# Optimization experiments

Hardware: AMD Instinct MI355X
Metric: run time of the kernel (lower is better)

The kernel has to match this reference:

```python
import jax, jax.numpy as jnp
import numpy as np

SWIGLU_ALPHA = 1.702
SWIGLU_LIMIT = 7.0
B, S, H, E, K, I = 2, 2048, 2048, 32, 4, 1024


def setup_inputs() -> dict:
    key = jax.random.key(0)
    ks = jax.random.split(key, 8)
    return {
        "hidden_states": jax.random.normal(ks[0], (B, S, H), jnp.float32),
        "gate_w": jax.random.normal(ks[1], (E, H), jnp.float32) * 0.02,
        "gate_b": jnp.zeros((E,), jnp.float32),
        "w_gate": jax.random.normal(ks[2], (E, H, I), jnp.float32) * 0.02,
        "b_gate": jnp.zeros((E, I), jnp.float32),
        "w_up": jax.random.normal(ks[3], (E, H, I), jnp.float32) * 0.02,
        "b_up": jnp.zeros((E, I), jnp.float32),
        "w_down": jax.random.normal(ks[4], (E, I, H), jnp.float32) * 0.02,
        "b_down": jnp.zeros((E, H), jnp.float32),
    }


def reference(hidden_states, gate_w, gate_b, w_gate, b_gate, w_up, b_up, w_down, b_down):
    Bb, Ss, Hh = hidden_states.shape
    x = hidden_states.reshape(-1, Hh)                      # [T, H]
    # --- gate: top-k logits first, then softmax over the selected subset ---
    logits = x @ gate_w.T + gate_b                         # [T, E]
    topk_logits, topk_idx = jax.lax.top_k(logits, K)       # sorted descending
    topk_weight = jax.nn.softmax(topk_logits.astype(jnp.float32), axis=-1)  # [T, K]
    # --- dispatch: replicate each token K times, sort by expert id ---
    flat_idx = topk_idx.reshape(-1)                        # [T*K]
    xs = jnp.repeat(x, K, axis=0)                          # [T*K, H]
    order = jnp.argsort(flat_idx)                          # stable sort by expert
    xt = xs[order]
    gid = flat_idx[order]                                  # expert id per sorted row
    group_sizes = jnp.bincount(flat_idx, length=E).astype(jnp.int32)
    # --- grouped GEMM experts with GPT-OSS SwiGLU ---
    gate = jax.lax.ragged_dot(xt, w_gate, group_sizes) + b_gate[gid]
    up = jax.lax.ragged_dot(xt, w_up, group_sizes) + b_up[gid]
    gate = jnp.minimum(gate, SWIGLU_LIMIT)
    up = jnp.clip(up, -SWIGLU_LIMIT, SWIGLU_LIMIT)
    glu = gate * jax.nn.sigmoid(SWIGLU_ALPHA * gate)
    activated = (up + 1.0) * glu
    outs = jax.lax.ragged_dot(activated, w_down, group_sizes) + b_down[gid]
    # --- unsort and combine with routing weights ---
    inv = jnp.argsort(order)
    outs = outs[inv].reshape(-1, K, Hh)                    # [T, K, H]
    y = jnp.sum(outs * topk_weight[..., None], axis=1).astype(x.dtype)
    return y.reshape(Bb, Ss, Hh)
```

## Files before the change

### kernel.cpp

```cpp
#include <hip/hip_runtime.h>

#define T_TOK 4096
#define E_EXP 32
#define HDIM  2048
#define IDIM  1024
#define TKROW 16384
#define BM    256
#define MAXT  96

typedef __attribute__((ext_vector_type(8))) short   short8;
typedef __attribute__((ext_vector_type(8))) __bf16  bf16x8;
typedef __attribute__((ext_vector_type(4))) float   f32x4;

typedef const __attribute__((address_space(1))) unsigned int* gas_t;
typedef __attribute__((address_space(3))) unsigned int*       las_t;

static __device__ __forceinline__ void gload16(const void* g, void* l) {
    __builtin_amdgcn_global_load_lds((gas_t)(uintptr_t)g, (las_t)(uintptr_t)l, 16, 0, 0);
}

static __device__ __forceinline__ f32x4 mfma16(short8 a, short8 b, f32x4 c) {
    return __builtin_amdgcn_mfma_f32_16x16x32_bf16(
        __builtin_bit_cast(bf16x8, a), __builtin_bit_cast(bf16x8, b), c, 0, 0, 0);
}

static __device__ __forceinline__ unsigned short f2bf(float f) {
    unsigned u = __builtin_bit_cast(unsigned, f);
    unsigned r = (u + 0x7FFFu + ((u >> 16) & 1u)) >> 16;
    return (unsigned short)r;
}
static __device__ __forceinline__ float bf2f(unsigned short u) {
    return __builtin_bit_cast(float, ((unsigned)u) << 16);
}
static __device__ __forceinline__ unsigned cvtpk(float lo, float hi) {
    unsigned r;
    asm("v_cvt_pk_bf16_f32 %0, %1, %2" : "=v"(r) : "v"(lo), "v"(hi));
    return r;
}

#define VM0()   asm volatile("s_waitcnt vmcnt(0)" ::: "memory")
#define LGKM0() asm volatile("s_waitcnt lgkmcnt(0)" ::: "memory")

__global__ __launch_bounds__(256) void gating_kernel(
    const float* __restrict__ x, const float* __restrict__ gw,
    const float* __restrict__ gb, int* __restrict__ topk_idx,
    float* __restrict__ topk_w)
{
    int wave = threadIdx.x >> 6, lane = threadIdx.x & 63;
    int t = blockIdx.x * 4 + wave;
    const float* xr = x + (size_t)t * HDIM;
    float xv[32];
#pragma unroll
    for (int j = 0; j < 32; j++) xv[j] = xr[lane + 64 * j];
    float logits[E_EXP];
#pragma unroll
    for (int e = 0; e < E_EXP; e++) {
        const float* wr = gw + (size_t)e * HDIM;
        float s = 0.f;
#pragma unroll
        for (int j = 0; j < 32; j++) s = fmaf(xv[j], wr[lane + 64 * j], s);
#pragma unroll
        for (int off = 32; off; off >>= 1) s += __shfl_xor(s, off);
        logits[e] = s + gb[e];
    }
    unsigned sel = 0;
    float v[4]; int id[4];
#pragma unroll
    for (int kk = 0; kk < 4; kk++) {
        float best = -3.4e38f; int bi = 0;
#pragma unroll
        for (int e = 0; e < E_EXP; e++) {
            bool ok = ((sel >> e) & 1u) == 0u;
            bool gt = ok && (logits[e] > best);
            best = gt ? logits[e] : best;
            bi   = gt ? e : bi;
        }
        sel |= 1u << bi; v[kk] = best; id[kk] = bi;
    }
    float m0 = v[0];
    float e0 = __expf(v[0] - m0), e1 = __expf(v[1] - m0);
    float e2 = __expf(v[2] - m0), e3 = __expf(v[3] - m0);
    float inv = 1.f / (e0 + e1 + e2 + e3);
    if (lane == 0) {
        int b4 = t * 4;
        topk_idx[b4 + 0] = id[0]; topk_w[b4 + 0] = e0 * inv;
        topk_idx[b4 + 1] = id[1]; topk_w[b4 + 1] = e1 * inv;
        topk_idx[b4 + 2] = id[2]; topk_w[b4 + 2] = e2 * inv;
        topk_idx[b4 + 3] = id[3]; topk_w[b4 + 3] = e3 * inv;
    }
}

__global__ void init_kernel(int* counts, int* fill) {
    if (threadIdx.x < E_EXP) { counts[threadIdx.x] = 0; fill[threadIdx.x] = 0; }
}

__global__ void histo_kernel(const int* __restrict__ idx, int* counts) {
    int i = blockIdx.x * 256 + threadIdx.x;
    atomicAdd(&counts[idx[i]], 1);
}

__global__ void scan_tiles_kernel(const int* counts, int* offsets,
                                  int* tile_e, int* tile_r, int* ntiles) {
    if (threadIdx.x == 0) {
        int acc = 0;
        for (int e = 0; e < E_EXP; e++) { offsets[e] = acc; acc += counts[e]; }
        offsets[E_EXP] = acc;
        int nt = 0;
        for (int e = 0; e < E_EXP; e++) {
            int c = counts[e];
            for (int r = 0; r < c; r += BM) {
                tile_e[nt] = e; tile_r[nt] = offsets[e] + r; nt++;
            }
        }
        ntiles[0] = nt;
    }
}

__global__ void scatter_kernel(const int* __restrict__ idx, const int* __restrict__ offsets,
                               int* fill, int* __restrict__ pos_of, int* __restrict__ row_tok) {
    int i = blockIdx.x * 256 + threadIdx.x;
    int e = idx[i];
    int pos = offsets[e] + atomicAdd(&fill[e], 1);
    pos_of[i] = pos;
    row_tok[pos] = i >> 2;
}

__global__ __launch_bounds__(64) void gather_kernel(
    const float* __restrict__ x, const int* __restrict__ row_tok,
    unsigned short* __restrict__ xt)
{
    int r = blockIdx.x, lane = threadIdx.x;
    const f32x4* src = (const f32x4*)(x + (size_t)row_tok[r] * HDIM);
    unsigned short* dst = xt + (size_t)r * HDIM;
#pragma unroll
    for (int j = 0; j < 8; j++) {
        f32x4 f = src[lane + 64 * j];
        uint2 o;
        o.x = cvtpk(f[0], f[1]);
        o.y = cvtpk(f[2], f[3]);
        *(uint2*)(dst + 4 * (lane + 64 * j)) = o;
    }
}

__global__ __launch_bounds__(512, 2) void gemm1_kernel(
    const unsigned short* __restrict__ xt, const float* __restrict__ w_gate,
    const float* __restrict__ b_gate, const float* __restrict__ w_up,
    const float* __restrict__ b_up, const int* __restrict__ tile_e,
    const int* __restrict__ tile_r, const int* __restrict__ ntiles,
    const int* __restrict__ offsets, const int* __restrict__ counts,
    unsigned short* __restrict__ act)
{
    __shared__ unsigned short As[2][BM * 64];
    __shared__ unsigned short Bgs[2][128 * 64];
    __shared__ unsigned short Bus[2][128 * 64];

    int t = threadIdx.x, lane = t & 63, w = t >> 6;
    int wr = w >> 2, wc = w & 3;
    int lrow = lane & 15, lg8 = (lane >> 4) * 8;

    int arow_l = (lane >> 3);
    int achunk = (lane & 7) ^ arow_l;
    int bn = (t & 31) * 4, bk = (t >> 5) * 4;
    int bfswz = ((t & 31) & 7) << 3;

    int nt = ntiles[0];
    int nitems = nt * 8;

    for (int item = blockIdx.x; item < nitems; item += gridDim.x) {
        int tid = item % nt, nb = item / nt;
        int e = tile_e[tid], row0 = tile_r[tid];
        int cnt_end = offsets[e] + counts[e];
        int n0 = nb * 128;

        f32x4 accg[8][2], accu[8][2];
#pragma unroll
        for (int m = 0; m < 8; m++)
#pragma unroll
            for (int n = 0; n < 2; n++) { accg[m][n] = (f32x4)0.f; accu[m][n] = (f32x4)0.f; }

        size_t wB = (size_t)e * ((size_t)HDIM * IDIM) + (size_t)bk * IDIM + n0 + bn;
        f32x4 gReg[4], uReg[4];

#define G1_STAGE_A(KT, BUF) do { int k0_ = (KT) * 64; \
    _Pragma("unroll") for (int i_ = 0; i_ < 4; i_++) { \
        int ar_ = row0 + 32 * w + 8 * i_ + arow_l; \
        if (ar_ > TKROW - 1) ar_ = TKROW - 1; \
        gload16(xt + (size_t)ar_ * HDIM + k0_ + achunk * 8, \
                (void*)&As[BUF][(32 * w + 8 * i_) * 64]); \
    } } while (0)

#define G1_LOADB(KT) do { \
    const float* gp_ = w_gate + wB + (size_t)(KT) * 64 * IDIM; \
    const float* up_ = w_up   + wB + (size_t)(KT) * 64 * IDIM; \
    _Pragma("unroll") for (int kk_ = 0; kk_ < 4; kk_++) { \
        gReg[kk_] = *(const f32x4*)(gp_ + (size_t)kk_ * IDIM); \
        uReg[kk_] = *(const f32x4*)(up_ + (size_t)kk_ * IDIM); \
    } } while (0)

#define G1_WRITEB(BUF) do { \
    _Pragma("unroll") for (int j_ = 0; j_ < 4; j_++) { \
        uint2 vg_, vu_; \
        vg_.x = cvtpk(gReg[0][j_], gReg[1][j_]); vg_.y = cvtpk(gReg[2][j_], gReg[3][j_]); \
        vu_.x = cvtpk(uReg[0][j_], uReg[1][j_]); vu_.y = cvtpk(uReg[2][j_], uReg[3][j_]); \
        int d_ = (bn + j_) * 64 + (bk ^ bfswz); \
        *(uint2*)&Bgs[BUF][d_] = vg_; *(uint2*)&Bus[BUF][d_] = vu_; \
    } } while (0)

#define G1_MFMA(BUF) do { \
    __builtin_amdgcn_s_setprio(1); \
    _Pragma("unroll") for (int kk_ = 0; kk_ < 2; kk_++) { \
        short8 af_[8], bg_[2], bu_[2]; \
        int ke_ = kk_ * 32 + lg8; \
        _Pragma("unroll") for (int m_ = 0; m_ < 8; m_++) \
            af_[m_] = *(const short8*)&As[BUF][(wr * 128 + m_ * 16 + lrow) * 64 + (ke_ ^ ((lrow & 7) << 3))]; \
        _Pragma("unroll") for (int n_ = 0; n_ < 2; n_++) { \
            int rb_ = wc * 32 + n_ * 16 + lrow; \
            int d_ = rb_ * 64 + (ke_ ^ (((rb_ >> 2) & 7) << 3)); \
            bg_[n_] = *(const short8*)&Bgs[BUF][d_]; \
            bu_[n_] = *(const short8*)&Bus[BUF][d_]; \
        } \
        _Pragma("unroll") for (int m_ = 0; m_ < 8; m_++) \
        _Pragma("unroll") for (int n_ = 0; n_ < 2; n_++) { \
            accg[m_][n_] = mfma16(af_[m_], bg_[n_], accg[m_][n_]); \
            accu[m_][n_] = mfma16(af_[m_], bu_[n_], accu[m_][n_]); \
        } \
    } \
    __builtin_amdgcn_s_setprio(0); } while (0)

        G1_STAGE_A(0, 0);
        G1_LOADB(0);
        VM0();
        G1_WRITEB(0);
        LGKM0();
        __builtin_amdgcn_s_barrier();

        int cur = 0;
#pragma unroll 1
        for (int kt = 0; kt < 32; kt++) {
            if (kt + 1 < 32) { G1_STAGE_A(kt + 1, cur ^ 1); G1_LOADB(kt + 1); }
            G1_MFMA(cur);
            VM0();
            if (kt + 1 < 32) G1_WRITEB(cur ^ 1);
            LGKM0();
            __builtin_amdgcn_s_barrier();
            cur ^= 1;
        }
#undef G1_STAGE_A
#undef G1_LOADB
#undef G1_WRITEB
#undef G1_MFMA

#pragma unroll
        for (int nf = 0; nf < 2; nf++) {
            int col = n0 + wc * 32 + nf * 16 + lrow;
            float bgv = b_gate[e * IDIM + col];
            float buv = b_up[e * IDIM + col];
#pragma unroll
            for (int m = 0; m < 8; m++) {
                int rb = row0 + wr * 128 + m * 16 + (lane >> 4) * 4;
#pragma unroll
                for (int r = 0; r < 4; r++) {
                    int grow = rb + r;
                    if (grow < cnt_end) {
                        float gv = accg[m][nf][r] + bgv;
                        float uv = accu[m][nf][r] + buv;
                        gv = fminf(gv, 7.f);
                        uv = fminf(fmaxf(uv, -7.f), 7.f);
                        float glu = gv / (1.f + __expf(-1.702f * gv));
                        act[(size_t)grow * IDIM + col] = f2bf((uv + 1.f) * glu);
                    }
                }
            }
        }
        __builtin_amdgcn_s_barrier();
    }
}

__global__ __launch_bounds__(512, 2) void gemm2_kernel(
    const unsigned short* __restrict__ actb, const float* __restrict__ w_down,
    const float* __restrict__ b_down, const int* __restrict__ tile_e,
    const int* __restrict__ tile_r, const int* __restrict__ ntiles,
    const int* __restrict__ offsets, const int* __restrict__ counts,
    unsigned short* __restrict__ outs)
{
    __shared__ unsigned short As[2][BM * 64];
    __shared__ unsigned short Bs[2][256 * 64];

    int t = threadIdx.x, lane = t & 63, w = t >> 6;
    int wr = w >> 2, wc = w & 3;
    int lrow = lane & 15, lg8 = (lane >> 4) * 8;

    int arow_l = (lane >> 3);
    int achunk = (lane & 7) ^ arow_l;
    int bn = (t & 63) * 4, bk = w * 8;
    int bfswz = (lane & 7) << 3;

    int nt = ntiles[0];
    int nitems = nt * 8;

    for (int item = blockIdx.x; item < nitems; item += gridDim.x) {
        int tid = item % nt, nb = item / nt;
        int e = tile_e[tid], row0 = tile_r[tid];
        int cnt_end = offsets[e] + counts[e];
        int n0 = nb * 256;

        f32x4 acc[8][4];
#pragma unroll
        for (int m = 0; m < 8; m++)
#pragma unroll
            for (int n = 0; n < 4; n++) acc[m][n] = (f32x4)0.f;

        size_t wB = (size_t)e * ((size_t)IDIM * HDIM) + (size_t)bk * HDIM + n0 + bn;
        f32x4 dReg[8];

#define G2_STAGE_A(KT, BUF) do { int k0_ = (KT) * 64; \
    _Pragma("unroll") for (int i_ = 0; i_ < 4; i_++) { \
        int ar_ = row0 + 32 * w + 8 * i_ + arow_l; \
        if (ar_ > TKROW - 1) ar_ = TKROW - 1; \
        gload16(actb + (size_t)ar_ * IDIM + k0_ + achunk * 8, \
                (void*)&As[BUF][(32 * w + 8 * i_) * 64]); \
    } } while (0)

#define G2_LOADB(KT) do { \
    const float* gp_ = w_down + wB + (size_t)(KT) * 64 * HDIM; \
    _Pragma("unroll") for (int kk_ = 0; kk_ < 8; kk_++) \
        dReg[kk_] = *(const f32x4*)(gp_ + (size_t)kk_ * HDIM); \
    } while (0)

#define G2_WRITEB(BUF) do { \
    _Pragma("unroll") for (int j_ = 0; j_ < 4; j_++) { \
        uint4 v_; \
        v_.x = cvtpk(dReg[0][j_], dReg[1][j_]); v_.y = cvtpk(dReg[2][j_], dReg[3][j_]); \
        v_.z = cvtpk(dReg[4][j_], dReg[5][j_]); v_.w = cvtpk(dReg[6][j_], dReg[7][j_]); \
        int d_ = (bn + j_) * 64 + (bk ^ bfswz); \
        *(uint4*)&Bs[BUF][d_] = v_; \
    } } while (0)

#define G2_MFMA(BUF) do { \
    __builtin_amdgcn_s_setprio(1); \
    _Pragma("unroll") for (int kk_ = 0; kk_ < 2; kk_++) { \
        short8 af_[8], bf_[4]; \
        int ke_ = kk_ * 32 + lg8; \
        _Pragma("unroll") for (int m_ = 0; m_ < 8; m_++) \
            af_[m_] = *(const short8*)&As[BUF][(wr * 128 + m_ * 16 + lrow) * 64 + (ke_ ^ ((lrow & 7) << 3))]; \
        _Pragma("unroll") for (int n_ = 0; n_ < 4; n_++) { \
            int rb_ = wc * 64 + n_ * 16 + lrow; \
            bf_[n_] = *(const short8*)&Bs[BUF][rb_ * 64 + (ke_ ^ (((rb_ >> 2) & 7) << 3))]; \
        } \
        _Pragma("unroll") for (int m_ = 0; m_ < 8; m_++) \
        _Pragma("unroll") for (int n_ = 0; n_ < 4; n_++) \
            acc[m_][n_] = mfma16(af_[m_], bf_[n_], acc[m_][n_]); \
    } \
    __builtin_amdgcn_s_setprio(0); } while (0)

        G2_STAGE_A(0, 0);
        G2_LOADB(0);
        VM0();
        G2_WRITEB(0);
        LGKM0();
        __builtin_amdgcn_s_barrier();

        int cur = 0;
#pragma unroll 1
        for (int kt = 0; kt < 16; kt++) {
            if (kt + 1 < 16) { G2_STAGE_A(kt + 1, cur ^ 1); G2_LOADB(kt + 1); }
            G2_MFMA(cur);
            VM0();
            if (kt + 1 < 16) G2_WRITEB(cur ^ 1);
            LGKM0();
            __builtin_amdgcn_s_barrier();
            cur ^= 1;
        }
#undef G2_STAGE_A
#undef G2_LOADB
#undef G2_WRITEB
#undef G2_MFMA

#pragma unroll
        for (int nf = 0; nf < 4; nf++) {
            int col = n0 + wc * 64 + nf * 16 + lrow;
            float bdv = b_down[e * HDIM + col];
#pragma unroll
            for (int m = 0; m < 8; m++) {
                int rb = row0 + wr * 128 + m * 16 + (lane >> 4) * 4;
#pragma unroll
                for (int r = 0; r < 4; r++) {
                    int grow = rb + r;
                    if (grow < cnt_end)
                        outs[(size_t)grow * HDIM + col] = f2bf(acc[m][nf][r] + bdv);
                }
            }
        }
        __builtin_amdgcn_s_barrier();
    }
}

__global__ __launch_bounds__(256) void combine_kernel(
    const unsigned short* __restrict__ outs, const int* __restrict__ pos_of,
    const float* __restrict__ topk_w, float* __restrict__ y)
{
    int tok = blockIdx.x;
    int c0 = threadIdx.x * 8;
    float acc[8] = {0.f, 0.f, 0.f, 0.f, 0.f, 0.f, 0.f, 0.f};
#pragma unroll
    for (int k = 0; k < 4; k++) {
        int pos = pos_of[tok * 4 + k];
        float w = topk_w[tok * 4 + k];
        short8 vv = *(const short8*)(outs + (size_t)pos * HDIM + c0);
#pragma unroll
        for (int j = 0; j < 8; j++)
            acc[j] = fmaf(w, bf2f((unsigned short)vv[j]), acc[j]);
    }
    float4 o0 = make_float4(acc[0], acc[1], acc[2], acc[3]);
    float4 o1 = make_float4(acc[4], acc[5], acc[6], acc[7]);
    *(float4*)(y + (size_t)tok * HDIM + c0)     = o0;
    *(float4*)(y + (size_t)tok * HDIM + c0 + 4) = o1;
}

extern "C" void kernel_launch(void* const* d_in, const int* in_sizes, int n_in,
                              void* d_out, int out_size, void* d_ws, size_t ws_size,
                              hipStream_t stream) {
    const float* x      = (const float*)d_in[0];
    const float* gw     = (const float*)d_in[1];
    const float* gb     = (const float*)d_in[2];
    const float* w_gate = (const float*)d_in[3];
    const float* b_gate = (const float*)d_in[4];
    const float* w_up   = (const float*)d_in[5];
    const float* b_up   = (const float*)d_in[6];
    const float* w_down = (const float*)d_in[7];
    const float* b_down = (const float*)d_in[8];
    float* y = (float*)d_out;

    char* base = (char*)d_ws;
    size_t off = 0;
    int*   topk_idx = (int*)(base + off);   off += (size_t)TKROW * 4;
    float* topk_w   = (float*)(base + off); off += (size_t)TKROW * 4;
    int*   counts   = (int*)(base + off);   off += 256;
    int*   offsets  = (int*)(base + off);   off += 256;
    int*   fill     = (int*)(base + off);   off += 256;
    int*   ntiles   = (int*)(base + off);   off += 256;
    int*   tile_e   = (int*)(base + off);   off += 1024;
    int*   tile_r   = (int*)(base + off);   off += 1024;
    int*   pos_of   = (int*)(base + off);   off += (size_t)TKROW * 4;
    int*   row_tok  = (int*)(base + off);   off += (size_t)TKROW * 4;
    unsigned short* xt   = (unsigned short*)(base + off); off += (size_t)TKROW * HDIM * 2;
    unsigned short* act  = (unsigned short*)(base + off); off += (size_t)TKROW * IDIM * 2;
    unsigned short* outs = (unsigned short*)(base + off); off += (size_t)TKROW * HDIM * 2;

    init_kernel<<<1, 64, 0, stream>>>(counts, fill);
    gating_kernel<<<T_TOK / 4, 256, 0, stream>>>(x, gw, gb, topk_idx, topk_w);
    histo_kernel<<<TKROW / 256, 256, 0, stream>>>(topk_idx, counts);
    scan_tiles_kernel<<<1, 64, 0, stream>>>(counts, offsets, tile_e, tile_r, ntiles);
    scatter_kernel<<<TKROW / 256, 256, 0, stream>>>(topk_idx, offsets, fill, pos_of, row_tok);
    gather_kernel<<<TKROW, 64, 0, stream>>>(x, row_tok, xt);
    gemm1_kernel<<<256, 512, 0, stream>>>(
        xt, w_gate, b_gate, w_up, b_up, tile_e, tile_r, ntiles, offsets, counts, act);
    gemm2_kernel<<<256, 512, 0, stream>>>(
        act, w_down, b_down, tile_e, tile_r, ntiles, offsets, counts, outs);
    combine_kernel<<<T_TOK, 256, 0, stream>>>(outs, pos_of, topk_w, y);
}
```

Measured before the change: 709.0 us.

## Replace persistent grid-stride GEMM loops with a precomputed XCD-aware worklist grid

```diff
diff --git a/kernel.cpp b/kernel.cpp
--- a/kernel.cpp
+++ b/kernel.cpp
@@ -7,6 +7,7 @@
 #define TKROW 16384
 #define BM    256
 #define MAXT  96
+#define WLY   160
 
 typedef __attribute__((ext_vector_type(8))) short   short8;
 typedef __attribute__((ext_vector_type(8))) __bf16  bf16x8;
@@ -100,19 +101,39 @@
 }
 
 __global__ void scan_tiles_kernel(const int* counts, int* offsets,
-                                  int* tile_e, int* tile_r, int* ntiles) {
-    if (threadIdx.x == 0) {
+                                  int* tile_e, int* tile_r, int* ntiles, int* wl) {
+    int t = threadIdx.x;
+    for (int i = t; i < 8 * WLY; i += 64) wl[i] = -1;
+    __syncthreads();
+    if (t == 0) {
         int acc = 0;
+        int tstart[E_EXP + 1];
         for (int e = 0; e < E_EXP; e++) { offsets[e] = acc; acc += counts[e]; }
         offsets[E_EXP] = acc;
         int nt = 0;
         for (int e = 0; e < E_EXP; e++) {
+            tstart[e] = nt;
             int c = counts[e];
             for (int r = 0; r < c; r += BM) {
                 tile_e[nt] = e; tile_r[nt] = offsets[e] + r; nt++;
             }
         }
+        tstart[E_EXP] = nt;
         ntiles[0] = nt;
+        int cnt[8];
+        for (int i = 0; i < 8; i++) cnt[i] = 0;
+        for (int nb = 0; nb < 8; nb++) {
+            for (int e = 0; e < E_EXP; e++) {
+                int ntl = tstart[e + 1] - tstart[e];
+                if (ntl == 0) continue;
+                int best = 0;
+                for (int xc = 1; xc < 8; xc++) if (cnt[xc] < cnt[best]) best = xc;
+                for (int k = 0; k < ntl && cnt[best] < WLY; k++) {
+                    wl[cnt[best] * 8 + best] = ((tstart[e] + k) << 3) | nb;
+                    cnt[best]++;
+                }
+            }
+        }
     }
 }
 
@@ -146,10 +167,17 @@
     const unsigned short* __restrict__ xt, const float* __restrict__ w_gate,
     const float* __restrict__ b_gate, const float* __restrict__ w_up,
     const float* __restrict__ b_up, const int* __restrict__ tile_e,
-    const int* __restrict__ tile_r, const int* __restrict__ ntiles,
+    const int* __restrict__ tile_r, const int* __restrict__ wl,
     const int* __restrict__ offsets, const int* __restrict__ counts,
     unsigned short* __restrict__ act)
 {
+    int item = wl[blockIdx.y * 8 + blockIdx.x];
+    if (item < 0) return;
+    int tid = item >> 3, nb = item & 7;
+    int e = tile_e[tid], row0 = tile_r[tid];
+    int cnt_end = offsets[e] + counts[e];
+    int n0 = nb * 128;
+
     __shared__ unsigned short As[2][BM * 64];
     __shared__ unsigned short Bgs[2][128 * 64];
     __shared__ unsigned short Bus[2][128 * 64];
@@ -157,29 +185,20 @@
     int t = threadIdx.x, lane = t & 63, w = t >> 6;
     int wr = w >> 2, wc = w & 3;
     int lrow = lane & 15, lg8 = (lane >> 4) * 8;
+
+    f32x4 accg[8][2], accu[8][2];
+#pragma unroll
+    for (int m = 0; m < 8; m++)
+#pragma unroll
+        for (int n = 0; n < 2; n++) { accg[m][n] = (f32x4)0.f; accu[m][n] = (f32x4)0.f; }
 
     int arow_l = (lane >> 3);
     int achunk = (lane & 7) ^ arow_l;
     int bn = (t & 31) * 4, bk = (t >> 5) * 4;
     int bfswz = ((t & 31) & 7) << 3;
-
-    int nt = ntiles[0];
-    int nitems = nt * 8;
-
-    for (int item = blockIdx.x; item < nitems; item += gridDim.x) {
-        int tid = item % nt, nb = item / nt;
-        int e = tile_e[tid], row0 = tile_r[tid];
-        int cnt_end = offsets[e] + counts[e];
-        int n0 = nb * 128;
-
-        f32x4 accg[8][2], accu[8][2];
-#pragma unroll
-        for (int m = 0; m < 8; m++)
-#pragma unroll
-            for (int n = 0; n < 2; n++) { accg[m][n] = (f32x4)0.f; accu[m][n] = (f32x4)0.f; }
-
-        size_t wB = (size_t)e * ((size_t)HDIM * IDIM) + (size_t)bk * IDIM + n0 + bn;
-        f32x4 gReg[4], uReg[4];
+    size_t wB = (size_t)e * ((size_t)HDIM * IDIM) + (size_t)bk * IDIM + n0 + bn;
+
+    f32x4 gReg[4], uReg[4];
 
 #define G1_STAGE_A(KT, BUF) do { int k0_ = (KT) * 64; \
     _Pragma("unroll") for (int i_ = 0; i_ < 4; i_++) { \
@@ -227,91 +246,87 @@
     } \
     __builtin_amdgcn_s_setprio(0); } while (0)
 
-        G1_STAGE_A(0, 0);
-        G1_LOADB(0);
+    G1_STAGE_A(0, 0);
+    G1_LOADB(0);
+    VM0();
+    G1_WRITEB(0);
+    LGKM0();
+    __builtin_amdgcn_s_barrier();
+
+    int cur = 0;
+#pragma unroll 1
+    for (int kt = 0; kt < 32; kt++) {
+        if (kt + 1 < 32) { G1_STAGE_A(kt + 1, cur ^ 1); G1_LOADB(kt + 1); }
+        G1_MFMA(cur);
         VM0();
-        G1_WRITEB(0);
+        if (kt + 1 < 32) G1_WRITEB(cur ^ 1);
         LGKM0();
         __builtin_amdgcn_s_barrier();
-
-        int cur = 0;
-#pragma unroll 1
-        for (int kt = 0; kt < 32; kt++) {
-            if (kt + 1 < 32) { G1_STAGE_A(kt + 1, cur ^ 1); G1_LOADB(kt + 1); }
-            G1_MFMA(cur);
-            VM0();
-            if (kt + 1 < 32) G1_WRITEB(cur ^ 1);
-            LGKM0();
-            __builtin_amdgcn_s_barrier();
-            cur ^= 1;
-        }
+        cur ^= 1;
+    }
 #undef G1_STAGE_A
 #undef G1_LOADB
 #undef G1_WRITEB
 #undef G1_MFMA
 
 #pragma unroll
-        for (int nf = 0; nf < 2; nf++) {
-            int col = n0 + wc * 32 + nf * 16 + lrow;
-            float bgv = b_gate[e * IDIM + col];
-            float buv = b_up[e * IDIM + col];
-#pragma unroll
-            for (int m = 0; m < 8; m++) {
-                int rb = row0 + wr * 128 + m * 16 + (lane >> 4) * 4;
-#pragma unroll
-                for (int r = 0; r < 4; r++) {
-                    int grow = rb + r;
-                    if (grow < cnt_end) {
-                        float gv = accg[m][nf][r] + bgv;
-                        float uv = accu[m][nf][r] + buv;
-                        gv = fminf(gv, 7.f);
-                        uv = fminf(fmaxf(uv, -7.f), 7.f);
-                        float glu = gv / (1.f + __expf(-1.702f * gv));
-                        act[(size_t)grow * IDIM + col] = f2bf((uv + 1.f) * glu);
-                    }
+    for (int nf = 0; nf < 2; nf++) {
+        int col = n0 + wc * 32 + nf * 16 + lrow;
+        float bgv = b_gate[e * IDIM + col];
+        float buv = b_up[e * IDIM + col];
+#pragma unroll
+        for (int m = 0; m < 8; m++) {
+            int rb = row0 + wr * 128 + m * 16 + (lane >> 4) * 4;
+#pragma unroll
+            for (int r = 0; r < 4; r++) {
+                int grow = rb + r;
+                if (grow < cnt_end) {
+                    float gv = accg[m][nf][r] + bgv;
+                    float uv = accu[m][nf][r] + buv;
+                    gv = fminf(gv, 7.f);
+                    uv = fminf(fmaxf(uv, -7.f), 7.f);
+                    float glu = gv / (1.f + __expf(-1.702f * gv));
+                    act[(size_t)grow * IDIM + col] = f2bf((uv + 1.f) * glu);
                 }
             }
         }
-        __builtin_amdgcn_s_barrier();
     }
 }
 
 __global__ __launch_bounds__(512, 2) void gemm2_kernel(
     const unsigned short* __restrict__ actb, const float* __restrict__ w_down,
     const float* __restrict__ b_down, const int* __restrict__ tile_e,
-    const int* __restrict__ tile_r, const int* __restrict__ ntiles,
+    const int* __restrict__ tile_r, const int* __restrict__ wl,
     const int* __restrict__ offsets, const int* __restrict__ counts,
     unsigned short* __restrict__ outs)
 {
+    int item = wl[blockIdx.y * 8 + blockIdx.x];
+    if (item < 0) return;
+    int tid = item >> 3, nb = item & 7;
+    int e = tile_e[tid], row0 = tile_r[tid];
+    int cnt_end = offsets[e] + counts[e];
+    int n0 = nb * 256;
+
     __shared__ unsigned short As[2][BM * 64];
     __shared__ unsigned short Bs[2][256 * 64];
 
     int t = threadIdx.x, lane = t & 63, w = t >> 6;
     int wr = w >> 2, wc = w & 3;
     int lrow = lane & 15, lg8 = (lane >> 4) * 8;
+
+    f32x4 acc[8][4];
+#pragma unroll
+    for (int m = 0; m < 8; m++)
+#pragma unroll
+        for (int n = 0; n < 4; n++) acc[m][n] = (f32x4)0.f;
 
     int arow_l = (lane >> 3);
     int achunk = (lane & 7) ^ arow_l;
     int bn = (t & 63) * 4, bk = w * 8;
     int bfswz = (lane & 7) << 3;
-
-    int nt = ntiles[0];
-    int nitems = nt * 8;
-
-    for (int item = blockIdx.x; item < nitems; item += gridDim.x) {
-        int tid = item % nt, nb = item / nt;
-        int e = tile_e[tid], row0 = tile_r[tid];
-        int cnt_end = offsets[e] + counts[e];
-        int n0 = nb * 256;
-
-        f32x4 acc[8][4];
-#pragma unroll
-        for (int m = 0; m < 8; m++)
-#pragma unroll
-            for (int n = 0; n < 4; n++) acc[m][n] = (f32x4)0.f;
-
-        size_t wB = (size_t)e * ((size_t)IDIM * HDIM) + (size_t)bk * HDIM + n0 + bn;
-        f32x4 dReg[8];
+    size_t wB = (size_t)e * ((size_t)IDIM * HDIM) + (size_t)bk * HDIM + n0 + bn;
+
+    f32x4 dReg[8];
 
 #define G2_STAGE_A(KT, BUF) do { int k0_ = (KT) * 64; \
     _Pragma("unroll") for (int i_ = 0; i_ < 4; i_++) { \
@@ -353,45 +368,43 @@
     } \
     __builtin_amdgcn_s_setprio(0); } while (0)
 
-        G2_STAGE_A(0, 0);
-        G2_LOADB(0);
+    G2_STAGE_A(0, 0);
+    G2_LOADB(0);
+    VM0();
+    G2_WRITEB(0);
+    LGKM0();
+    __builtin_amdgcn_s_barrier();
+
+    int cur = 0;
+#pragma unroll 1
+    for (int kt = 0; kt < 16; kt++) {
+        if (kt + 1 < 16) { G2_STAGE_A(kt + 1, cur ^ 1); G2_LOADB(kt + 1); }
+        G2_MFMA(cur);
         VM0();
-        G2_WRITEB(0);
+        if (kt + 1 < 16) G2_WRITEB(cur ^ 1);
         LGKM0();
         __builtin_amdgcn_s_barrier();
-
-        int cur = 0;
-#pragma unroll 1
-        for (int kt = 0; kt < 16; kt++) {
-            if (kt + 1 < 16) { G2_STAGE_A(kt + 1, cur ^ 1); G2_LOADB(kt + 1); }
-            G2_MFMA(cur);
-            VM0();
-            if (kt + 1 < 16) G2_WRITEB(cur ^ 1);
-            LGKM0();
-            __builtin_amdgcn_s_barrier();
-            cur ^= 1;
-        }
+        cur ^= 1;
+    }
 #undef G2_STAGE_A
 #undef G2_LOADB
 #undef G2_WRITEB
 #undef G2_MFMA
 
 #pragma unroll
-        for (int nf = 0; nf < 4; nf++) {
-            int col = n0 + wc * 64 + nf * 16 + lrow;
-            float bdv = b_down[e * HDIM + col];
-#pragma unroll
-            for (int m = 0; m < 8; m++) {
-                int rb = row0 + wr * 128 + m * 16 + (lane >> 4) * 4;
-#pragma unroll
-                for (int r = 0; r < 4; r++) {
-                    int grow = rb + r;
-                    if (grow < cnt_end)
-                        outs[(size_t)grow * HDIM + col] = f2bf(acc[m][nf][r] + bdv);
-                }
+    for (int nf = 0; nf < 4; nf++) {
+        int col = n0 + wc * 64 + nf * 16 + lrow;
+        float bdv = b_down[e * HDIM + col];
+#pragma unroll
+        for (int m = 0; m < 8; m++) {
+            int rb = row0 + wr * 128 + m * 16 + (lane >> 4) * 4;
+#pragma unroll
+            for (int r = 0; r < 4; r++) {
+                int grow = rb + r;
+                if (grow < cnt_end)
+                    outs[(size_t)grow * HDIM + col] = f2bf(acc[m][nf][r] + bdv);
             }
         }
-        __builtin_amdgcn_s_barrier();
     }
 }
 
@@ -441,6 +454,7 @@
     int*   ntiles   = (int*)(base + off);   off += 256;
     int*   tile_e   = (int*)(base + off);   off += 1024;
     int*   tile_r   = (int*)(base + off);   off += 1024;
+    int*   wl       = (int*)(base + off);   off += (size_t)8 * WLY * 4;
     int*   pos_of   = (int*)(base + off);   off += (size_t)TKROW * 4;
     int*   row_tok  = (int*)(base + off);   off += (size_t)TKROW * 4;
     unsigned short* xt   = (unsigned short*)(base + off); off += (size_t)TKROW * HDIM * 2;
@@ -450,12 +464,12 @@
     init_kernel<<<1, 64, 0, stream>>>(counts, fill);
     gating_kernel<<<T_TOK / 4, 256, 0, stream>>>(x, gw, gb, topk_idx, topk_w);
     histo_kernel<<<TKROW / 256, 256, 0, stream>>>(topk_idx, counts);
-    scan_tiles_kernel<<<1, 64, 0, stream>>>(counts, offsets, tile_e, tile_r, ntiles);
+    scan_tiles_kernel<<<1, 64, 0, stream>>>(counts, offsets, tile_e, tile_r, ntiles, wl);
     scatter_kernel<<<TKROW / 256, 256, 0, stream>>>(topk_idx, offsets, fill, pos_of, row_tok);
     gather_kernel<<<TKROW, 64, 0, stream>>>(x, row_tok, xt);
-    gemm1_kernel<<<256, 512, 0, stream>>>(
-        xt, w_gate, b_gate, w_up, b_up, tile_e, tile_r, ntiles, offsets, counts, act);
-    gemm2_kernel<<<256, 512, 0, stream>>>(
-        act, w_down, b_down, tile_e, tile_r, ntiles, offsets, counts, outs);
+    gemm1_kernel<<<dim3(8, WLY), 512, 0, stream>>>(
+        xt, w_gate, b_gate, w_up, b_up, tile_e, tile_r, wl, offsets, counts, act);
+    gemm2_kernel<<<dim3(8, WLY), 512, 0, stream>>>(
+        act, w_down, b_down, tile_e, tile_r, wl, offsets, counts, outs);
     combine_kernel<<<T_TOK, 256, 0, stream>>>(outs, pos_of, topk_w, y);
 }
```

Result: slower. 741.7 us (+4.6%).
